# Optimization experiments

Hardware: AMD Instinct MI355X
Metric: run time of the kernel (lower is better)

Reference implementation:

```python
import jax, jax.numpy as jnp
import numpy as np

TOKENS = 32768
DIM = 2048
N_EXPERTS = 64
TOP_K = 6
ROUTE_SCALE = 1.0


def setup_inputs() -> dict:
    key = jax.random.key(0)
    k1, k2, k3 = jax.random.split(key, 3)
    x = jax.random.normal(k1, (TOKENS, DIM), dtype=jnp.float32)
    weight = jax.random.normal(k2, (N_EXPERTS, DIM), dtype=jnp.float32) * (1.0 / np.sqrt(DIM))
    bias = jax.random.normal(k3, (N_EXPERTS,), dtype=jnp.float32) * 0.01
    return {"x": x, "weight": weight, "bias": bias}


def reference(x, weight, bias):
    # scores = F.linear(x, weight): [T, E]
    logits = jnp.einsum('td,ed->te', x, weight)
    # softmax in float32 (score_func == 'softmax')
    original_scores = jax.nn.softmax(logits.astype(jnp.float32), axis=-1)
    # bias only affects expert selection, not the returned weights
    biased = original_scores + bias
    _, indices = jax.lax.top_k(biased, TOP_K)  # [T, top_k]
    weights = jnp.take_along_axis(original_scores, indices, axis=-1)
    weights = weights * ROUTE_SCALE
    return weights.astype(x.dtype), indices
```

## Files before the change

### kernel.cpp

```cpp
#include <hip/hip_runtime.h>
#include <hip/hip_bf16.h>
#include <math.h>

#define TOKENS 32768
#define DIM    2048
#define NEXP   64
#define TOPK   6

#define BM   64
#define BK   64
#define NIT  (DIM / BK)
#define ST   72
#define PLANE (BM * ST)

typedef float f32x4 __attribute__((ext_vector_type(4)));
typedef short sh8  __attribute__((ext_vector_type(8)));

__device__ __forceinline__ ushort f2bf(float f) {
    union { __hip_bfloat16 b; ushort u; } c;
    c.b = __float2bfloat16(f);
    return c.u;
}
__device__ __forceinline__ float bf2f(ushort u) {
    union { ushort u; __hip_bfloat16 b; } c;
    c.u = u;
    return __bfloat162float(c.b);
}

__global__ __launch_bounds__(256, 2)
void gate_kernel(const float* __restrict__ x,
                 const float* __restrict__ w,
                 const float* __restrict__ bias,
                 float* __restrict__ out)
{
    __shared__ __align__(16) short smem[6 * PLANE];

    const int tid  = threadIdx.x;
    const int wave = tid >> 6;
    const int lane = tid & 63;
    const int quad = lane >> 4;
    const int l15  = lane & 15;
    const int tok0 = blockIdx.x * BM;

    const int sr = tid >> 2;
    const int sq = tid & 3;

    const float* xg = x + (long)(tok0 + sr) * DIM + sq * 16;
    const float* wg = w + (long)sr * DIM + sq * 16;

    f32x4 acc[4];
#pragma unroll
    for (int nt = 0; nt < 4; ++nt) acc[nt] = (f32x4){0.f, 0.f, 0.f, 0.f};

    float4 xf[4], wf[4];

    auto stage = [&]() {
        const int base = sr * ST + sq * 16;
#pragma unroll
        for (int g = 0; g < 2; ++g) {
            sh8 xh, xm, xl, wh, wm, wl;
#pragma unroll
            for (int i = 0; i < 8; ++i) {
                {
                    float f = ((const float*)&xf[g * 2])[i];
                    ushort h = f2bf(f);  float r1 = f - bf2f(h);
                    ushort m = f2bf(r1); float r2 = r1 - bf2f(m);
                    ushort l = f2bf(r2);
                    xh[i] = (short)h; xm[i] = (short)m; xl[i] = (short)l;
                }
                {
                    float f = ((const float*)&wf[g * 2])[i];
                    ushort h = f2bf(f);  float r1 = f - bf2f(h);
                    ushort m = f2bf(r1); float r2 = r1 - bf2f(m);
                    ushort l = f2bf(r2);
                    wh[i] = (short)h; wm[i] = (short)m; wl[i] = (short)l;
                }
            }
            *(sh8*)&smem[0 * PLANE + base + g * 8] = xh;
            *(sh8*)&smem[1 * PLANE + base + g * 8] = xm;
            *(sh8*)&smem[2 * PLANE + base + g * 8] = xl;
            *(sh8*)&smem[3 * PLANE + base + g * 8] = wh;
            *(sh8*)&smem[4 * PLANE + base + g * 8] = wm;
            *(sh8*)&smem[5 * PLANE + base + g * 8] = wl;
        }
    };

#pragma unroll
    for (int j = 0; j < 4; ++j) {
        xf[j] = *(const float4*)(xg + j * 4);
        wf[j] = *(const float4*)(wg + j * 4);
    }

    for (int it = 0; it < NIT; ++it) {
        stage();
        __syncthreads();

        if (it + 1 < NIT) {
            const int k0 = (it + 1) * BK;
#pragma unroll
            for (int j = 0; j < 4; ++j) {
                xf[j] = *(const float4*)(xg + k0 + j * 4);
                wf[j] = *(const float4*)(wg + k0 + j * 4);
            }
        }

        const int arow = (wave * 16 + l15) * ST;
#pragma unroll
        for (int ks = 0; ks < 2; ++ks) {
            const int kof = ks * 32 + quad * 8;
            sh8 ah = *(const sh8*)&smem[0 * PLANE + arow + kof];
            sh8 am = *(const sh8*)&smem[1 * PLANE + arow + kof];
            sh8 al = *(const sh8*)&smem[2 * PLANE + arow + kof];
#pragma unroll
            for (int nt = 0; nt < 4; ++nt) {
                const int brow = (nt * 16 + l15) * ST;
                sh8 bh = *(const sh8*)&smem[3 * PLANE + brow + kof];
                sh8 bm = *(const sh8*)&smem[4 * PLANE + brow + kof];
                sh8 bl = *(const sh8*)&smem[5 * PLANE + brow + kof];
                acc[nt] = __builtin_amdgcn_mfma_f32_16x16x32_bf16(ah, bh, acc[nt], 0, 0, 0);
                acc[nt] = __builtin_amdgcn_mfma_f32_16x16x32_bf16(am, bh, acc[nt], 0, 0, 0);
                acc[nt] = __builtin_amdgcn_mfma_f32_16x16x32_bf16(ah, bm, acc[nt], 0, 0, 0);
                acc[nt] = __builtin_amdgcn_mfma_f32_16x16x32_bf16(al, bh, acc[nt], 0, 0, 0);
                acc[nt] = __builtin_amdgcn_mfma_f32_16x16x32_bf16(am, bm, acc[nt], 0, 0, 0);
                acc[nt] = __builtin_amdgcn_mfma_f32_16x16x32_bf16(ah, bl, acc[nt], 0, 0, 0);
            }
        }
        __syncthreads();
    }

    float* red = (float*)smem;
#pragma unroll
    for (int nt = 0; nt < 4; ++nt)
#pragma unroll
        for (int j = 0; j < 4; ++j) {
            const int row = wave * 16 + quad * 4 + j;
            const int col = nt * 16 + l15;
            red[row * 69 + col] = acc[nt][j];
        }
    __syncthreads();

    if (tid < BM) {
        const int m = tid;
        float lg[NEXP];
#pragma unroll
        for (int e = 0; e < NEXP; ++e) lg[e] = red[m * 69 + e];

        float mx = lg[0];
#pragma unroll
        for (int e = 1; e < NEXP; ++e) mx = fmaxf(mx, lg[e]);

        float sc4[NEXP];
        float sum = 0.f;
#pragma unroll
        for (int e = 0; e < NEXP; ++e) { sc4[e] = __expf(lg[e] - mx); sum += sc4[e]; }
        const float inv = 1.0f / sum;

        float bz[NEXP];
#pragma unroll
        for (int e = 0; e < NEXP; ++e) {
            sc4[e] *= inv;
            bz[e]  = sc4[e] + bias[e];
        }

        const int tok = tok0 + m;
        float* wout = out + (long)tok * TOPK;
        float* iout = out + (long)TOKENS * TOPK + (long)tok * TOPK;

        int win[TOPK];
#pragma unroll
        for (int p = 0; p < TOPK; ++p) {
            float bmax = -INFINITY;
            int   best = 0;
            float bsc  = 0.f;
#pragma unroll
            for (int e = 0; e < NEXP; ++e) {
                bool skip = false;
#pragma unroll
                for (int pp = 0; pp < p; ++pp) skip = skip || (e == win[pp]);
                float v = skip ? -INFINITY : bz[e];
                if (v > bmax) { bmax = v; best = e; bsc = sc4[e]; }
            }
            win[p]  = best;
            wout[p] = bsc;
            iout[p] = (float)best;
        }
    }
}

extern "C" void kernel_launch(void* const* d_in, const int* in_sizes, int n_in,
                              void* d_out, int out_size, void* d_ws, size_t ws_size,
                              hipStream_t stream) {
    const float* x = (const float*)d_in[0];
    const float* w = (const float*)d_in[1];
    const float* b = (const float*)d_in[2];
    float* out = (float*)d_out;

    dim3 grid(TOKENS / BM);
    dim3 block(256);
    gate_kernel<<<grid, block, 0, stream>>>(x, w, b, out);
}
```

Before: 386.2 us.

## Pre-split weights into bf16 planes and feed MFMA straight from global memory

```diff
diff --git a/kernel.cpp b/kernel.cpp
--- a/kernel.cpp
+++ b/kernel.cpp
@@ -6,12 +6,7 @@
 #define DIM    2048
 #define NEXP   64
 #define TOPK   6
-
-#define BM   64
-#define BK   64
-#define NIT  (DIM / BK)
-#define ST   72
-#define PLANE (BM * ST)
+#define NKS    (DIM / 32)
 
 typedef float f32x4 __attribute__((ext_vector_type(4)));
 typedef short sh8  __attribute__((ext_vector_type(8)));
@@ -27,119 +22,158 @@
     return __bfloat162float(c.b);
 }
 
+__global__ __launch_bounds__(256)
+void wsplit_kernel(const float* __restrict__ w,
+                   short* __restrict__ wh, short* __restrict__ wm,
+                   short* __restrict__ wl)
+{
+    const int i = (blockIdx.x * 256 + threadIdx.x) * 4;
+    float4 f4 = *(const float4*)(w + i);
+    short h4[4], m4[4], l4[4];
+#pragma unroll
+    for (int j = 0; j < 4; ++j) {
+        float f = ((const float*)&f4)[j];
+        ushort h = f2bf(f);  float r1 = f - bf2f(h);
+        ushort m = f2bf(r1); float r2 = r1 - bf2f(m);
+        h4[j] = (short)h; m4[j] = (short)m; l4[j] = (short)f2bf(r2);
+    }
+    *(short4*)(wh + i) = *(short4*)h4;
+    *(short4*)(wm + i) = *(short4*)m4;
+    *(short4*)(wl + i) = *(short4*)l4;
+}
+
 __global__ __launch_bounds__(256, 2)
 void gate_kernel(const float* __restrict__ x,
-                 const float* __restrict__ w,
+                 const short* __restrict__ wh,
+                 const short* __restrict__ wm,
+                 const short* __restrict__ wl,
                  const float* __restrict__ bias,
                  float* __restrict__ out)
 {
-    __shared__ __align__(16) short smem[6 * PLANE];
+    __shared__ float red[64 * 69];
 
     const int tid  = threadIdx.x;
     const int wave = tid >> 6;
     const int lane = tid & 63;
     const int quad = lane >> 4;
     const int l15  = lane & 15;
-    const int tok0 = blockIdx.x * BM;
-
-    const int sr = tid >> 2;
-    const int sq = tid & 3;
-
-    const float* xg = x + (long)(tok0 + sr) * DIM + sq * 16;
-    const float* wg = w + (long)sr * DIM + sq * 16;
-
-    f32x4 acc[4];
-#pragma unroll
-    for (int nt = 0; nt < 4; ++nt) acc[nt] = (f32x4){0.f, 0.f, 0.f, 0.f};
-
-    float4 xf[4], wf[4];
-
-    auto stage = [&]() {
-        const int base = sr * ST + sq * 16;
-#pragma unroll
-        for (int g = 0; g < 2; ++g) {
-            sh8 xh, xm, xl, wh, wm, wl;
+    const int tg   = wave >> 1;
+    const int eg   = wave & 1;
+    const int tok0 = blockIdx.x * 64;
+
+    const float* xr[2];
+#pragma unroll
+    for (int mt = 0; mt < 2; ++mt)
+        xr[mt] = x + (long)(tok0 + tg * 32 + mt * 16 + l15) * DIM + quad * 8;
+
+    long brow[2];
+#pragma unroll
+    for (int nt = 0; nt < 2; ++nt)
+        brow[nt] = (long)(eg * 32 + nt * 16 + l15) * DIM + quad * 8;
+
+    f32x4 acc[2][2];
+#pragma unroll
+    for (int mt = 0; mt < 2; ++mt)
+#pragma unroll
+        for (int nt = 0; nt < 2; ++nt)
+            acc[mt][nt] = (f32x4){0.f, 0.f, 0.f, 0.f};
+
+    f32x4 xa[2][2];
+    sh8 nbh[2], nbm[2], nbl[2];
+
+#pragma unroll
+    for (int mt = 0; mt < 2; ++mt) {
+        xa[mt][0] = *(const f32x4*)(xr[mt]);
+        xa[mt][1] = *(const f32x4*)(xr[mt] + 4);
+    }
+#pragma unroll
+    for (int nt = 0; nt < 2; ++nt) {
+        nbh[nt] = *(const sh8*)(wh + brow[nt]);
+        nbm[nt] = *(const sh8*)(wm + brow[nt]);
+        nbl[nt] = *(const sh8*)(wl + brow[nt]);
+    }
+
+#pragma unroll 2
+    for (int ks = 0; ks < NKS; ++ks) {
+        f32x4 ca[2][2];
+        sh8 cbh[2], cbm[2], cbl[2];
+#pragma unroll
+        for (int mt = 0; mt < 2; ++mt) { ca[mt][0] = xa[mt][0]; ca[mt][1] = xa[mt][1]; }
+#pragma unroll
+        for (int nt = 0; nt < 2; ++nt) { cbh[nt] = nbh[nt]; cbm[nt] = nbm[nt]; cbl[nt] = nbl[nt]; }
+
+        if (ks + 1 < NKS) {
+            const int k0 = (ks + 1) * 32;
+#pragma unroll
+            for (int mt = 0; mt < 2; ++mt) {
+                xa[mt][0] = *(const f32x4*)(xr[mt] + k0);
+                xa[mt][1] = *(const f32x4*)(xr[mt] + k0 + 4);
+            }
+#pragma unroll
+            for (int nt = 0; nt < 2; ++nt) {
+                nbh[nt] = *(const sh8*)(wh + brow[nt] + k0);
+                nbm[nt] = *(const sh8*)(wm + brow[nt] + k0);
+                nbl[nt] = *(const sh8*)(wl + brow[nt] + k0);
+            }
+        }
+
+        sh8 ah[2], am[2], al[2];
+#pragma unroll
+        for (int mt = 0; mt < 2; ++mt) {
 #pragma unroll
             for (int i = 0; i < 8; ++i) {
-                {
-                    float f = ((const float*)&xf[g * 2])[i];
-                    ushort h = f2bf(f);  float r1 = f - bf2f(h);
-                    ushort m = f2bf(r1); float r2 = r1 - bf2f(m);
-                    ushort l = f2bf(r2);
-                    xh[i] = (short)h; xm[i] = (short)m; xl[i] = (short)l;
-                }
-                {
-                    float f = ((const float*)&wf[g * 2])[i];
-                    ushort h = f2bf(f);  float r1 = f - bf2f(h);
-                    ushort m = f2bf(r1); float r2 = r1 - bf2f(m);
-                    ushort l = f2bf(r2);
-                    wh[i] = (short)h; wm[i] = (short)m; wl[i] = (short)l;
-                }
-            }
-            *(sh8*)&smem[0 * PLANE + base + g * 8] = xh;
-            *(sh8*)&smem[1 * PLANE + base + g * 8] = xm;
-            *(sh8*)&smem[2 * PLANE + base + g * 8] = xl;
-            *(sh8*)&smem[3 * PLANE + base + g * 8] = wh;
-            *(sh8*)&smem[4 * PLANE + base + g * 8] = wm;
-            *(sh8*)&smem[5 * PLANE + base + g * 8] = wl;
-        }
-    };
-
-#pragma unroll
-    for (int j = 0; j < 4; ++j) {
-        xf[j] = *(const float4*)(xg + j * 4);
-        wf[j] = *(const float4*)(wg + j * 4);
-    }
-
-    for (int it = 0; it < NIT; ++it) {
-        stage();
-        __syncthreads();
-
-        if (it + 1 < NIT) {
-            const int k0 = (it + 1) * BK;
+                float f = ((const float*)&ca[mt][i >> 2])[i & 3];
+                ushort h = f2bf(f);  float r1 = f - bf2f(h);
+                ushort m = f2bf(r1); float r2 = r1 - bf2f(m);
+                ah[mt][i] = (short)h; am[mt][i] = (short)m; al[mt][i] = (short)f2bf(r2);
+            }
+        }
+
+#pragma unroll
+        for (int mt = 0; mt < 2; ++mt)
+#pragma unroll
+            for (int nt = 0; nt < 2; ++nt)
+                acc[mt][nt] = __builtin_amdgcn_mfma_f32_16x16x32_bf16(ah[mt], cbh[nt], acc[mt][nt], 0, 0, 0);
+#pragma unroll
+        for (int mt = 0; mt < 2; ++mt)
+#pragma unroll
+            for (int nt = 0; nt < 2; ++nt)
+                acc[mt][nt] = __builtin_amdgcn_mfma_f32_16x16x32_bf16(am[mt], cbh[nt], acc[mt][nt], 0, 0, 0);
+#pragma unroll
+        for (int mt = 0; mt < 2; ++mt)
+#pragma unroll
+            for (int nt = 0; nt < 2; ++nt)
+                acc[mt][nt] = __builtin_amdgcn_mfma_f32_16x16x32_bf16(ah[mt], cbm[nt], acc[mt][nt], 0, 0, 0);
+#pragma unroll
+        for (int mt = 0; mt < 2; ++mt)
+#pragma unroll
+            for (int nt = 0; nt < 2; ++nt)
+                acc[mt][nt] = __builtin_amdgcn_mfma_f32_16x16x32_bf16(al[mt], cbh[nt], acc[mt][nt], 0, 0, 0);
+#pragma unroll
+        for (int mt = 0; mt < 2; ++mt)
+#pragma unroll
+            for (int nt = 0; nt < 2; ++nt)
+                acc[mt][nt] = __builtin_amdgcn_mfma_f32_16x16x32_bf16(am[mt], cbm[nt], acc[mt][nt], 0, 0, 0);
+#pragma unroll
+        for (int mt = 0; mt < 2; ++mt)
+#pragma unroll
+            for (int nt = 0; nt < 2; ++nt)
+                acc[mt][nt] = __builtin_amdgcn_mfma_f32_16x16x32_bf16(ah[mt], cbl[nt], acc[mt][nt], 0, 0, 0);
+    }
+
+#pragma unroll
+    for (int mt = 0; mt < 2; ++mt)
+#pragma unroll
+        for (int nt = 0; nt < 2; ++nt)
 #pragma unroll
             for (int j = 0; j < 4; ++j) {
-                xf[j] = *(const float4*)(xg + k0 + j * 4);
-                wf[j] = *(const float4*)(wg + k0 + j * 4);
-            }
-        }
-
-        const int arow = (wave * 16 + l15) * ST;
-#pragma unroll
-        for (int ks = 0; ks < 2; ++ks) {
-            const int kof = ks * 32 + quad * 8;
-            sh8 ah = *(const sh8*)&smem[0 * PLANE + arow + kof];
-            sh8 am = *(const sh8*)&smem[1 * PLANE + arow + kof];
-            sh8 al = *(const sh8*)&smem[2 * PLANE + arow + kof];
-#pragma unroll
-            for (int nt = 0; nt < 4; ++nt) {
-                const int brow = (nt * 16 + l15) * ST;
-                sh8 bh = *(const sh8*)&smem[3 * PLANE + brow + kof];
-                sh8 bm = *(const sh8*)&smem[4 * PLANE + brow + kof];
-                sh8 bl = *(const sh8*)&smem[5 * PLANE + brow + kof];
-                acc[nt] = __builtin_amdgcn_mfma_f32_16x16x32_bf16(ah, bh, acc[nt], 0, 0, 0);
-                acc[nt] = __builtin_amdgcn_mfma_f32_16x16x32_bf16(am, bh, acc[nt], 0, 0, 0);
-                acc[nt] = __builtin_amdgcn_mfma_f32_16x16x32_bf16(ah, bm, acc[nt], 0, 0, 0);
-                acc[nt] = __builtin_amdgcn_mfma_f32_16x16x32_bf16(al, bh, acc[nt], 0, 0, 0);
-                acc[nt] = __builtin_amdgcn_mfma_f32_16x16x32_bf16(am, bm, acc[nt], 0, 0, 0);
-                acc[nt] = __builtin_amdgcn_mfma_f32_16x16x32_bf16(ah, bl, acc[nt], 0, 0, 0);
-            }
-        }
-        __syncthreads();
-    }
-
-    float* red = (float*)smem;
-#pragma unroll
-    for (int nt = 0; nt < 4; ++nt)
-#pragma unroll
-        for (int j = 0; j < 4; ++j) {
-            const int row = wave * 16 + quad * 4 + j;
-            const int col = nt * 16 + l15;
-            red[row * 69 + col] = acc[nt][j];
-        }
+                const int row = tg * 32 + mt * 16 + quad * 4 + j;
+                const int col = eg * 32 + nt * 16 + l15;
+                red[row * 69 + col] = acc[mt][nt][j];
+            }
     __syncthreads();
 
-    if (tid < BM) {
+    if (tid < 64) {
         const int m = tid;
         float lg[NEXP];
 #pragma unroll
@@ -195,7 +229,10 @@
     const float* b = (const float*)d_in[2];
     float* out = (float*)d_out;
 
-    dim3 grid(TOKENS / BM);
-    dim3 block(256);
-    gate_kernel<<<grid, block, 0, stream>>>(x, w, b, out);
-}
+    short* wh = (short*)d_ws;
+    short* wm = wh + NEXP * DIM;
+    short* wl = wm + NEXP * DIM;
+
+    wsplit_kernel<<<dim3(NEXP * DIM / (256 * 4)), dim3(256), 0, stream>>>(w, wh, wm, wl);
+    gate_kernel<<<dim3(TOKENS / 64), dim3(256), 0, stream>>>(x, wh, wm, wl, b, out);
+}
```

After: 458.3 us. 1.19x slower.
